# Optimization experiments

Measured on AMD Instinct MI355X. Metric: run time of the kernel, lower is better.

Reference implementation:

```python
import jax, jax.numpy as jnp
import numpy as np

EPS = 1e-6

def _ln(x, g, b):
    mu = x.mean(-1, keepdims=True)
    var = ((x - mu) ** 2).mean(-1, keepdims=True)
    return (x - mu) * jax.lax.rsqrt(var + EPS) * g + b

def _ln_l2_grad(z, target, g, b):
    # grad of 0.5*||LN(z)*g+b - target||^2 wrt z (fused L2/LayerNorm backward used by TTT)
    d = z.shape[-1]
    mu = z.mean(-1, keepdims=True)
    var = ((z - mu) ** 2).mean(-1, keepdims=True)
    std = jnp.sqrt(var + EPS)
    zh = (z - mu) / std
    go = (zh * g + b) - target
    gxh = go * g
    return (d * gxh - gxh.sum(-1, keepdims=True) - zh * (gxh * zh).sum(-1, keepdims=True)) / (d * std)

def _forward(x, W_down, b_down, Wq, Wk, Wv, Wo, W1, b1, ttt_g, ttt_b,
             lr_w, lr_b, post_g, post_b, norm_g, norm_b, W_up, b_up):
    B, S, D = x.shape
    A = W_down.shape[1]
    H, hd, _ = W1.shape
    # adapter down projection + SiLU
    h = jax.nn.silu(x @ W_down + b_down)                      # [B,S,A]
    # TTT-Linear: q/k/v projections split into heads
    xq = (h @ Wq).reshape(B, S, H, hd)
    xk = (h @ Wk).reshape(B, S, H, hd)
    xv = (h @ Wv).reshape(B, S, H, hd)
    eta = jax.nn.sigmoid(h @ lr_w + lr_b) / hd                # [B,S,H] token-wise learnable inner lr (base_lr=1)
    W1_0 = jnp.broadcast_to(W1, (B, H, hd, hd))
    b1_0 = jnp.broadcast_to(b1, (B, H, 1, hd))
    xs = (xq.transpose(1, 0, 2, 3), xk.transpose(1, 0, 2, 3),
          xv.transpose(1, 0, 2, 3), eta.transpose(1, 0, 2))

    def step(carry, ins):
        W, bb = carry                                         # [B,H,hd,hd], [B,H,1,hd]
        q, k, v, e = ins                                      # [B,H,hd] x3, [B,H]
        Z = jnp.einsum('bhd,bhde->bhe', k, W) + bb[:, :, 0, :]
        g = _ln_l2_grad(Z, v - k, ttt_g, ttt_b)               # inner-loop grad wrt pre-LN activations
        e4 = e[:, :, None, None]
        Wn = W - e4 * (k[..., :, None] * g[..., None, :])     # fast-weight SGD update
        bn = bb - e4 * g[:, :, None, :]
        Zq = jnp.einsum('bhd,bhde->bhe', q, Wn) + bn[:, :, 0, :]
        out = q + _ln(Zq, ttt_g, ttt_b)                       # per-head TTT post residual
        return (Wn, bn), out

    _, ys = jax.lax.scan(step, (W1_0, b1_0), xs)              # ys: [S,B,H,hd]
    t = ys.transpose(1, 0, 2, 3).reshape(B, S, A)
    t = _ln(t, post_g, post_b) @ Wo                           # TTT post-norm + output projection
    out = _ln(t, norm_g, norm_b)                              # adapter LayerNorm
    return out @ W_up + b_up                                  # adapter up projection (residual unused in source)

def setup_inputs() -> dict:
    key = jax.random.key(0)
    ks = jax.random.split(key, 12)
    B, S, D, A, H = 4, 1024, 768, 192, 3
    hd = A // H
    s = 0.02
    return {
        'x': jax.random.normal(ks[0], (B, S, D), jnp.float32),
        'W_down': jax.random.normal(ks[1], (D, A), jnp.float32) * s,
        'b_down': jnp.zeros((A,), jnp.float32),
        'Wq': jax.random.normal(ks[2], (A, A), jnp.float32) * s,
        'Wk': jax.random.normal(ks[3], (A, A), jnp.float32) * s,
        'Wv': jax.random.normal(ks[4], (A, A), jnp.float32) * s,
        'Wo': jax.random.normal(ks[5], (A, A), jnp.float32) * s,
        'W1': jax.random.normal(ks[6], (H, hd, hd), jnp.float32) * s,
        'b1': jnp.zeros((H, 1, hd), jnp.float32),
        'ttt_g': jnp.ones((H, hd), jnp.float32),
        'ttt_b': jnp.zeros((H, hd), jnp.float32),
        'lr_w': jax.random.normal(ks[7], (A, H), jnp.float32) * s,
        'lr_b': jnp.zeros((H,), jnp.float32),
        'post_g': jnp.ones((A,), jnp.float32),
        'post_b': jnp.zeros((A,), jnp.float32),
        'norm_g': jnp.ones((A,), jnp.float32),
        'norm_b': jnp.zeros((A,), jnp.float32),
        'W_up': jax.random.normal(ks[8], (A, D), jnp.float32) * s,
        'b_up': jnp.zeros((D,), jnp.float32),
    }

def reference(x, W_down, b_down, Wq, Wk, Wv, Wo, W1, b1, ttt_g, ttt_b,
              lr_w, lr_b, post_g, post_b, norm_g, norm_b, W_up, b_up):
    return _forward(x, W_down, b_down, Wq, Wk, Wv, Wo, W1, b1, ttt_g, ttt_b,
                    lr_w, lr_b, post_g, post_b, norm_g, norm_b, W_up, b_up)
```

## Files before the change

kernel.cpp:

```cpp
#include <hip/hip_runtime.h>
#include <hip/hip_bf16.h>
#include <math.h>

#define BDIM 4
#define SDIM 1024
#define DDIM 768
#define ADIM 192
#define HDIM 3
#define HD   64
#define MROWS (BDIM*SDIM)
#define NCHUNK (SDIM/32)
#define EPSLN 1e-6f

template<int CTRL, int RMASK, bool BC>
__device__ __forceinline__ float dpp_add_step(float x) {
    int t = __builtin_amdgcn_update_dpp(0, __float_as_int(x), CTRL, RMASK, 0xf, BC);
    return x + __int_as_float(t);
}
__device__ __forceinline__ float wave_bcast_sum(float x) {
    x = dpp_add_step<0x111, 0xf, true >(x);
    x = dpp_add_step<0x112, 0xf, true >(x);
    x = dpp_add_step<0x114, 0xf, true >(x);
    x = dpp_add_step<0x118, 0xf, true >(x);
    x = dpp_add_step<0x142, 0xa, false>(x);
    x = dpp_add_step<0x143, 0xc, false>(x);
    return __int_as_float(__builtin_amdgcn_readlane(__float_as_int(x), 63));
}
__device__ __forceinline__ float dpp_row16_sum(float x) {
    x = dpp_add_step<0x111, 0xf, true >(x);
    x = dpp_add_step<0x112, 0xf, true >(x);
    x = dpp_add_step<0x114, 0xf, true >(x);
    x = dpp_add_step<0x118, 0xf, true >(x);
    return x;
}
__device__ __forceinline__ float rl(float v, int lane) {
    return __int_as_float(__builtin_amdgcn_readlane(__float_as_int(v), lane));
}
__device__ __forceinline__ float fast_rsq(float x) {
    float r;
    asm("v_rsq_f32 %0, %1" : "=v"(r) : "v"(x));
    return r;
}
__device__ __forceinline__ void red5_asm(float& a, float& b, float& c,
                                         float& d, float& e) {
#define R5_SHR(N)                                                              \
    asm("v_add_f32 %0, %0, %0 row_shr:" #N " row_mask:0xf bank_mask:0xf bound_ctrl:0" : "+v"(a)); \
    asm("v_add_f32 %0, %0, %0 row_shr:" #N " row_mask:0xf bank_mask:0xf bound_ctrl:0" : "+v"(b)); \
    asm("v_add_f32 %0, %0, %0 row_shr:" #N " row_mask:0xf bank_mask:0xf bound_ctrl:0" : "+v"(c)); \
    asm("v_add_f32 %0, %0, %0 row_shr:" #N " row_mask:0xf bank_mask:0xf bound_ctrl:0" : "+v"(d)); \
    asm("v_add_f32 %0, %0, %0 row_shr:" #N " row_mask:0xf bank_mask:0xf bound_ctrl:0" : "+v"(e));
#define R5_BC(N, RM)                                                           \
    asm("v_add_f32 %0, %0, %0 row_bcast:" #N " row_mask:" #RM " bank_mask:0xf" : "+v"(a)); \
    asm("v_add_f32 %0, %0, %0 row_bcast:" #N " row_mask:" #RM " bank_mask:0xf" : "+v"(b)); \
    asm("v_add_f32 %0, %0, %0 row_bcast:" #N " row_mask:" #RM " bank_mask:0xf" : "+v"(c)); \
    asm("v_add_f32 %0, %0, %0 row_bcast:" #N " row_mask:" #RM " bank_mask:0xf" : "+v"(d)); \
    asm("v_add_f32 %0, %0, %0 row_bcast:" #N " row_mask:" #RM " bank_mask:0xf" : "+v"(e));
    R5_SHR(1) R5_SHR(2) R5_SHR(4) R5_SHR(8)
    R5_BC(15, 0xa) R5_BC(31, 0xc)
#undef R5_SHR
#undef R5_BC
}

template<int ACT, int LAYOUT, int LNA, int STATS>
__global__ __launch_bounds__(256) void gemm_k(
    const float* __restrict__ A, const float* __restrict__ Bm,
    const float* __restrict__ bias, float* __restrict__ C,
    int M, int N, int K,
    const float2* __restrict__ lnst, const float* __restrict__ lng,
    const float* __restrict__ lnbb, float2* __restrict__ ostat)
{
    __shared__ float As[16][68];
    __shared__ float Bs[16][68];
    __shared__ float2 lst[64];
    const int tid = threadIdx.x;
    const int bm = blockIdx.y * 64, bn = blockIdx.x * 64;
    const int tr = tid >> 4, tc = tid & 15;
    float acc[4][4] = {};

    if (LNA == 2) {
        if (tid < 64) {
            float2 s = lnst[bm + tid];
            float mu = s.x * (1.f / 192.f);
            float var = fmaf(-mu, mu, s.y * (1.f / 192.f));
            lst[tid] = make_float2(mu, rsqrtf(var + EPSLN));
        }
        __syncthreads();
    }

    for (int k0 = 0; k0 < K; k0 += 16) {
        #pragma unroll
        for (int p = 0; p < 4; ++p) {
            int m = (tid >> 4) + p * 16;
            int kk = tid & 15;
            float av = A[(size_t)(bm + m) * K + k0 + kk];
            if (LNA == 2) {
                float2 stv = lst[m];
                av = fmaf((av - stv.x) * stv.y, lng[k0 + kk], lnbb[k0 + kk]);
            }
            As[kk][m] = av;
        }
        #pragma unroll
        for (int p = 0; p < 4; ++p) {
            int kk = (tid >> 6) + p * 4;
            int n = tid & 63;
            Bs[kk][n] = Bm[(size_t)(k0 + kk) * N + bn + n];
        }
        __syncthreads();
        #pragma unroll
        for (int kk = 0; kk < 16; ++kk) {
            const float4 a4 = *(const float4*)&As[kk][tr * 4];
            const float4 b4 = *(const float4*)&Bs[kk][tc * 4];
            float aa[4] = {a4.x, a4.y, a4.z, a4.w};
            float bb[4] = {b4.x, b4.y, b4.z, b4.w};
            #pragma unroll
            for (int i = 0; i < 4; ++i)
                #pragma unroll
                for (int j = 0; j < 4; ++j)
                    acc[i][j] = fmaf(aa[i], bb[j], acc[i][j]);
        }
        __syncthreads();
    }

    float rs1[4] = {}, rs2[4] = {};
    #pragma unroll
    for (int i = 0; i < 4; ++i) {
        int m = bm + tr * 4 + i;
        #pragma unroll
        for (int j = 0; j < 4; ++j) {
            int n = bn + tc * 4 + j;
            float v = acc[i][j];
            if (bias) v += bias[n];
            if (ACT == 1) v = v / (1.f + __expf(-v));
            if (STATS) { rs1[i] += v; rs2[i] = fmaf(v, v, rs2[i]); }
            if (LAYOUT == 0) {
                C[(size_t)m * N + n] = v;
            } else {
                int b  = m >> 10, s = m & 1023;
                int hh = n >> 6,  d = n & 63;
                C[(((size_t)b * HDIM + hh) * SDIM + s) * HD + d] = v;
            }
        }
    }
    if (STATS) {
        #pragma unroll
        for (int i = 0; i < 4; ++i) {
            rs1[i] = dpp_row16_sum(rs1[i]);
            rs2[i] = dpp_row16_sum(rs2[i]);
        }
        if (tc == 15) {
            #pragma unroll
            for (int i = 0; i < 4; ++i) {
                atomicAdd(&ostat[bm + tr * 4 + i].x, rs1[i]);
                atomicAdd(&ostat[bm + tr * 4 + i].y, rs2[i]);
            }
        }
    }
}

__global__ __launch_bounds__(256) void gemm_qkv(
    const float* __restrict__ A, const float* __restrict__ BWq,
    const float* __restrict__ BWk, const float* __restrict__ BWv,
    float* __restrict__ Cbase)
{
    const float* Bm = (blockIdx.z == 0) ? BWq : (blockIdx.z == 1) ? BWk : BWv;
    float* C = Cbase + (size_t)blockIdx.z * ((size_t)MROWS * ADIM);
    __shared__ float As[16][68];
    __shared__ float Bs[16][68];
    const int tid = threadIdx.x;
    const int bm = blockIdx.y * 64, bn = blockIdx.x * 64;
    const int tr = tid >> 4, tc = tid & 15;
    float acc[4][4] = {};

    for (int k0 = 0; k0 < ADIM; k0 += 16) {
        #pragma unroll
        for (int p = 0; p < 4; ++p) {
            int m = (tid >> 4) + p * 16;
            int kk = tid & 15;
            As[kk][m] = A[(size_t)(bm + m) * ADIM + k0 + kk];
        }
        #pragma unroll
        for (int p = 0; p < 4; ++p) {
            int kk = (tid >> 6) + p * 4;
            int n = tid & 63;
            Bs[kk][n] = Bm[(size_t)(k0 + kk) * ADIM + bn + n];
        }
        __syncthreads();
        #pragma unroll
        for (int kk = 0; kk < 16; ++kk) {
            const float4 a4 = *(const float4*)&As[kk][tr * 4];
            const float4 b4 = *(const float4*)&Bs[kk][tc * 4];
            float aa[4] = {a4.x, a4.y, a4.z, a4.w};
            float bb[4] = {b4.x, b4.y, b4.z, b4.w};
            #pragma unroll
            for (int i = 0; i < 4; ++i)
                #pragma unroll
                for (int j = 0; j < 4; ++j)
                    acc[i][j] = fmaf(aa[i], bb[j], acc[i][j]);
        }
        __syncthreads();
    }

    #pragma unroll
    for (int i = 0; i < 4; ++i) {
        int m = bm + tr * 4 + i;
        #pragma unroll
        for (int j = 0; j < 4; ++j) {
            int n = bn + tc * 4 + j;
            int b  = m >> 10, s = m & 1023;
            int hh = n >> 6,  d = n & 63;
            C[(((size_t)b * HDIM + hh) * SDIM + s) * HD + d] = acc[i][j];
        }
    }
}

__global__ __launch_bounds__(256) void ab_kernel(
    const float* __restrict__ qb, const float* __restrict__ kb,
    float* __restrict__ vb,
    const float* __restrict__ ttt_g, const float* __restrict__ ttt_b,
    float* __restrict__ Ab, float* __restrict__ Bb,
    float* __restrict__ r6b,
    const float* __restrict__ h, const float* __restrict__ lr_w,
    const float* __restrict__ lr_b, float* __restrict__ etab,
    float4* __restrict__ stz)
{
    int bh = blockIdx.x >> 5, c = blockIdx.x & 31, cs = c * 32;
    int hh = bh % HDIM, b = bh / HDIM;
    __shared__ float Kc[32][65], Qc[32][65], Vc[32][65];
    __shared__ float ep[32][8];

    if (blockIdx.x < 16) {
        float4 z4; z4.x = z4.y = z4.z = z4.w = 0.f;
        stz[blockIdx.x * 256 + threadIdx.x] = z4;
    }

    {
        int rg = threadIdx.x >> 3, sl = threadIdx.x & 7;
        const float* hrow = h + ((size_t)b * SDIM + cs + rg) * ADIM + sl * 24;
        float esum = 0.f;
        #pragma unroll
        for (int jj = 0; jj < 24; ++jj)
            esum = fmaf(hrow[jj], lr_w[(sl * 24 + jj) * 3 + hh], esum);
        ep[rg][sl] = esum;
    }

    for (int i = threadIdx.x; i < 2048; i += 256) {
        int t = i >> 6, j = i & 63;
        Kc[t][j] = kb[((size_t)bh * SDIM + cs + t) * HD + j];
        Qc[t][j] = qb[((size_t)bh * SDIM + cs + t) * HD + j];
        Vc[t][j] = vb[((size_t)bh * SDIM + cs + t) * HD + j];
    }
    __syncthreads();

    if (threadIdx.x < 32) {
        int t = threadIdx.x;
        float acc = ((ep[t][0] + ep[t][1]) + (ep[t][2] + ep[t][3]))
                  + ((ep[t][4] + ep[t][5]) + (ep[t][6] + ep[t][7]))
                  + lr_b[hh];
        float e = 1.f / (1.f + __expf(-acc)) * (1.f / 64.f);
        etab[(size_t)bh * SDIM + cs + t] = e;
    }

    size_t base = ((size_t)(bh * NCHUNK + c)) * 1024;
    for (int e = threadIdx.x; e < 1024; e += 256) {
        int t = e >> 5, s = e & 31;
        float a = 1.f, bv = 1.f;
        #pragma unroll
        for (int j = 0; j < 64; ++j) {
            float ks = Kc[s][j];
            a  = fmaf(Kc[t][j], ks, a);
            bv = fmaf(Qc[t][j], ks, bv);
        }
        Ab[base + e] = a;
        Bb[base + e] = bv;
    }
    for (int i = threadIdx.x; i < 2048; i += 256) {
        int t = i >> 6, j = i & 63;
        float gwv = ttt_g[hh * 64 + j], bwv = ttt_b[hh * 64 + j];
        float av = fmaf(-(Vc[t][j] - Kc[t][j]), gwv, bwv * gwv);
        Vc[t][j] = av;
        vb[((size_t)bh * SDIM + cs + t) * HD + j] = av;
    }
    __syncthreads();
    if (threadIdx.x < 32) {
        int t = threadIdx.x;
        float acc = 0.f;
        #pragma unroll
        for (int j = 0; j < 64; ++j) acc += Vc[t][j];
        r6b[(size_t)bh * SDIM + cs + t] = acc;
    }
}

__device__ __forceinline__ void stage_chunk(
    int pp, int cc, int bh, int idx, int nth,
    const float* __restrict__ kbuf, const float* __restrict__ abuf,
    const float* __restrict__ Ab, const float* __restrict__ etab,
    const float* __restrict__ r6b,
    float4* K4, float4* a4, float4* A4, float2* er6)
{
    const float4* kg = (const float4*)(kbuf + ((size_t)bh * SDIM + cc * 32) * HD);
    const float4* ag = (const float4*)(abuf + ((size_t)bh * SDIM + cc * 32) * HD);
    const float4* Ag = (const float4*)(Ab + ((size_t)(bh * NCHUNK + cc)) * 1024);
    for (int i = idx; i < 512; i += nth) K4[pp * 512 + i] = kg[i];
    for (int i = idx; i < 512; i += nth) a4[pp * 512 + i] = ag[i];
    for (int i = idx; i < 256; i += nth) A4[pp * 256 + i] = Ag[i];
    for (int i = idx; i < 32; i += nth)
        er6[pp * 32 + i] = make_float2(
            etab[(size_t)bh * SDIM + cc * 32 + i] * (1.f / 64.f),
            r6b[(size_t)bh * SDIM + cc * 32 + i]);
}

__global__ __launch_bounds__(256, 1) void ttt_scan(
    const float* __restrict__ kbuf, const float* __restrict__ abuf,
    const float* __restrict__ etab, const float* __restrict__ Ab,
    const float* __restrict__ r6b,
    const float* __restrict__ W1,   const float* __restrict__ b1,
    const float* __restrict__ ttt_g, const float* __restrict__ ttt_b,
    float* __restrict__ Gbuf, float* __restrict__ W0save, float* __restrict__ b0save)
{
    const int bh = blockIdx.x, hh = bh % HDIM;
    const int tid = threadIdx.x, lane = tid & 63;
    const int wv = tid >> 6;
    __shared__ float  Zp[4][16][64];
    __shared__ float4 K4s[2 * 512];
    __shared__ float4 a4s[2 * 512];
    __shared__ float4 A4s[2 * 256];
    __shared__ float2 er6s[2 * 32];
    __shared__ float  Gl[16][64];

    float Wreg[16];
    #pragma unroll
    for (int r = 0; r < 16; ++r)
        Wreg[r] = W1[hh * 4096 + (wv * 16 + r) * 64 + lane];
    float breg = b1[hh * 64 + lane];
    const float gw = ttt_g[hh * 64 + lane];
    const float bw = ttt_b[hh * 64 + lane];
    const float w3 = gw * gw;
    (void)bw;
    const float Cg2 = wave_bcast_sum(w3);
    const float* a_f = (const float*)a4s;

    stage_chunk(0, 0, bh, tid, 256, kbuf, abuf, Ab, etab, r6b,
                K4s, a4s, A4s, er6s);
    __syncthreads();

    for (int c = 0; c < NCHUNK; ++c) {
        const int cs = c * 32;
        const int p = c & 1;

        {
            float* Wd = W0save + ((size_t)(bh * NCHUNK + c)) * 4096
                        + (wv * 16) * 64 + lane;
            #pragma unroll
            for (int r = 0; r < 16; ++r) Wd[r * 64] = Wreg[r];
            if (tid < 64) b0save[(bh * NCHUNK + c) * 64 + tid] = breg;
        }

        #pragma unroll
        for (int h = 0; h < 2; ++h) {
            const int h16 = h * 16, h4 = h * 4;

            float Zt[16];
            #pragma unroll
            for (int i = 0; i < 16; ++i) {
                const int t = h16 + i;
                float zt = 0.f;
                #pragma unroll
                for (int r4 = 0; r4 < 4; ++r4) {
                    const float4 kv = K4s[p * 512 + t * 16 + wv * 4 + r4];
                    zt = fmaf(kv.x, Wreg[r4 * 4 + 0], zt);
                    zt = fmaf(kv.y, Wreg[r4 * 4 + 1], zt);
                    zt = fmaf(kv.z, Wreg[r4 * 4 + 2], zt);
                    zt = fmaf(kv.w, Wreg[r4 * 4 + 3], zt);
                }
                Zt[i] = zt;
            }
            if (wv != 0) {
                #pragma unroll
                for (int i = 0; i < 16; ++i)
                    Zp[wv][i][lane] = (wv == 1) ? Zt[i] + breg : Zt[i];
            }
            __syncthreads();

            if (wv == 0) {
                __builtin_amdgcn_s_setprio(1);
                float Z[16];
                #pragma unroll
                for (int i = 0; i < 16; ++i) {
                    float q1 = Zp[1][i][lane], q2 = Zp[2][i][lane],
                          q3 = Zp[3][i][lane];
                    Z[i] = ((Zt[i] + q1) + (q2 + q3));
                }
                float4 avA[4], avB[4];
                float aA, aB; float2 erA, erB;
                #pragma unroll
                for (int q = 0; q < 4; ++q)
                    avA[q] = A4s[p * 256 + h16 * 8 + h4 + q];
                aA  = a_f[p * 2048 + h16 * 64 + lane];
                erA = er6s[p * 32 + h16];
#define TOK(I, avC, aC, erC, avN, aN, erN)                                     \
    {                                                                          \
        if ((I) < 15) {                                                        \
            _Pragma("unroll")                                                  \
            for (int q = ((I) + 2) >> 2; q < 4; ++q)                           \
                avN[q] = A4s[p * 256 + (h16 + (I) + 1) * 8 + h4 + q];          \
            aN  = a_f[p * 2048 + (h16 + (I) + 1) * 64 + lane];                 \
            erN = er6s[p * 32 + h16 + (I) + 1];                                \
        }                                                                      \
        float z  = Z[I];                                                       \
        float a  = aC;                                                         \
        float zg = z * w3;                                                     \
        float x1 = z, x2 = z * z, x3 = zg, x4 = zg * z, x5 = z * a;            \
        red5_asm(x1, x2, x3, x4, x5);                                          \
        float r1 = rl(x1, 63), r2 = rl(x2, 63), r3 = rl(x3, 63);               \
        float r4 = rl(x4, 63), r5 = rl(x5, 63);                                \
        float r6t = (erC).y;                                                   \
        float mu   = r1 * (1.f / 64.f);                                        \
        float var  = fmaf(-mu, mu, r2 * (1.f / 64.f));                         \
        float rstd = fast_rsq(var + EPSLN);                                    \
        float mc   = mu * Cg2;                                                 \
        float sgxh = fmaf(rstd, r3 - mc, r6t);                                 \
        float t4v  = fmaf(mu, mc, fmaf(-2.f * mu, r3, r4));                    \
        float sgz  = fmaf(rstd * rstd, t4v, rstd * (r5 - mu * r6t));           \
        float zh   = (z - mu) * rstd;                                          \
        float gxh  = fmaf(zh, w3, a);                                          \
        float ge   = (fmaf(64.f, gxh, -sgxh) - zh * sgz) * (rstd * (erC).x);   \
        Gl[I][lane] = ge;                                                      \
        _Pragma("unroll")                                                      \
        for (int u = (I) + 1; u < 16; ++u) {                                   \
            const float4 c4 = avC[(u) >> 2]; const int m4 = (u) & 3;           \
            float Atu = (m4 == 0) ? c4.x : (m4 == 1) ? c4.y                    \
                      : (m4 == 2) ? c4.z : c4.w;                               \
            Z[u] = fmaf(-Atu, ge, Z[u]);                                       \
        }                                                                      \
    }
                #pragma unroll
                for (int tp = 0; tp < 8; ++tp) {
                    TOK(2 * tp,     avA, aA, erA, avB, aB, erB)
                    TOK(2 * tp + 1, avB, aB, erB, avA, aA, erA)
                }
#undef TOK
                __builtin_amdgcn_s_setprio(0);
            } else if (h == 0 && c < NCHUNK - 1) {
                stage_chunk(p ^ 1, c + 1, bh, tid - 64, 192,
                            kbuf, abuf, Ab, etab, r6b, K4s, a4s, A4s, er6s);
            }
            __syncthreads();

            float btot = 0.f;
            #pragma unroll
            for (int s = 0; s < 16; ++s) {
                float gd = Gl[s][lane];
                btot += gd;
                #pragma unroll
                for (int r4 = 0; r4 < 4; ++r4) {
                    const float4 kv = K4s[p * 512 + (h16 + s) * 16 + wv * 4 + r4];
                    Wreg[r4 * 4 + 0] = fmaf(-kv.x, gd, Wreg[r4 * 4 + 0]);
                    Wreg[r4 * 4 + 1] = fmaf(-kv.y, gd, Wreg[r4 * 4 + 1]);
                    Wreg[r4 * 4 + 2] = fmaf(-kv.z, gd, Wreg[r4 * 4 + 2]);
                    Wreg[r4 * 4 + 3] = fmaf(-kv.w, gd, Wreg[r4 * 4 + 3]);
                }
            }
            breg -= btot;
            {
                float* gb = Gbuf + ((size_t)bh * SDIM + cs + h16) * HD + lane;
                #pragma unroll
                for (int r = 0; r < 4; ++r)
                    gb[(wv * 4 + r) * HD] = Gl[wv * 4 + r][lane];
            }
        }
    }
}

__global__ __launch_bounds__(256) void post_kernel(
    const float* __restrict__ qbuf, const float* __restrict__ Bb,
    const float* __restrict__ Gbuf, const float* __restrict__ W0save,
    const float* __restrict__ b0save,
    const float* __restrict__ ttt_g, const float* __restrict__ ttt_b,
    float* __restrict__ ys, float2* __restrict__ ystat)
{
    const int bh = blockIdx.x >> 5, c = blockIdx.x & 31, cs = c * 32;
    const int b = bh / HDIM, hh = bh % HDIM;
    const int tid = threadIdx.x, lane = tid & 63, wave = tid >> 6;
    __shared__ float Qc[32][65];
    __shared__ float W0l[64][65];
    __shared__ float Gl[32][64];
    for (int i = tid; i < 2048; i += 256) {
        int t = i >> 6, j = i & 63;
        Qc[t][j] = qbuf[((size_t)bh * SDIM + cs + t) * HD + j];
        Gl[t][j] = Gbuf[((size_t)bh * SDIM + cs + t) * HD + j];
    }
    for (int i = tid; i < 4096; i += 256)
        W0l[i >> 6][i & 63] = W0save[((size_t)(bh * NCHUNK + c)) * 4096 + i];
    __syncthreads();

    const float bb0 = b0save[(bh * NCHUNK + c) * 64 + lane];
    const float gw = ttt_g[hh * 64 + lane], bw = ttt_b[hh * 64 + lane];
    float acc[8];
    #pragma unroll
    for (int r = 0; r < 8; ++r) acc[r] = bb0;
    for (int j = 0; j < 64; ++j) {
        float w0 = W0l[j][lane];
        #pragma unroll
        for (int r = 0; r < 8; ++r)
            acc[r] = fmaf(Qc[wave * 8 + r][j], w0, acc[r]);
    }
    float Breg[8];
    size_t bbase = ((size_t)(bh * NCHUNK + c)) * 1024;
    #pragma unroll
    for (int r = 0; r < 8; ++r)
        Breg[r] = Bb[bbase + (wave * 8 + r) * 32 + (lane & 31)];
    #pragma unroll
    for (int s = 0; s < 32; ++s) {
        float gd = Gl[s][lane];
        #pragma unroll
        for (int r = 0; r < 8; ++r) {
            int t = wave * 8 + r;
            float Bts = rl(Breg[r], s);
            acc[r] = (s <= t) ? fmaf(-Bts, gd, acc[r]) : acc[r];
        }
    }
    #pragma unroll
    for (int r = 0; r < 8; ++r) {
        int t = wave * 8 + r;
        float s1 = wave_bcast_sum(acc[r]);
        float s2 = wave_bcast_sum(acc[r] * acc[r]);
        float mu = s1 * (1.f / 64.f);
        float var = s2 * (1.f / 64.f) - mu * mu;
        float rstd = rsqrtf(var + EPSLN);
        float zh = (acc[r] - mu) * rstd;
        float val = zh * gw + bw + Qc[t][lane];
        ys[((size_t)(b * SDIM) + cs + t) * ADIM + hh * HD + lane] = val;
        float t1 = wave_bcast_sum(val);
        float t2 = wave_bcast_sum(val * val);
        if (lane == 0) {
            atomicAdd(&ystat[(size_t)b * SDIM + cs + t].x, t1);
            atomicAdd(&ystat[(size_t)b * SDIM + cs + t].y, t2);
        }
    }
}

extern "C" void kernel_launch(void* const* d_in, const int* in_sizes, int n_in,
                              void* d_out, int out_size, void* d_ws, size_t ws_size,
                              hipStream_t stream)
{
    const float* x      = (const float*)d_in[0];
    const float* W_down = (const float*)d_in[1];
    const float* b_down = (const float*)d_in[2];
    const float* Wq     = (const float*)d_in[3];
    const float* Wk     = (const float*)d_in[4];
    const float* Wv     = (const float*)d_in[5];
    const float* Wo     = (const float*)d_in[6];
    const float* W1     = (const float*)d_in[7];
    const float* b1     = (const float*)d_in[8];
    const float* ttt_g  = (const float*)d_in[9];
    const float* ttt_b  = (const float*)d_in[10];
    const float* lr_w   = (const float*)d_in[11];
    const float* lr_b   = (const float*)d_in[12];
    const float* post_g = (const float*)d_in[13];
    const float* post_b = (const float*)d_in[14];
    const float* norm_g = (const float*)d_in[15];
    const float* norm_b = (const float*)d_in[16];
    const float* W_up   = (const float*)d_in[17];
    const float* b_up   = (const float*)d_in[18];
    float* out = (float*)d_out;

    float* ws = (float*)d_ws;
    const size_t SZ = (size_t)MROWS * ADIM;
    float* h    = ws;
    float* qb   = ws + SZ;
    float* kb   = ws + 2 * SZ;
    float* vb   = ws + 3 * SZ;
    float* Gb   = ws + 4 * SZ;
    float* etab = ws + 5 * SZ;
    float* Ab   = etab + 12288;
    float* Bb   = Ab + 393216;
    float* W0s  = Bb + 393216;
    float* b0s  = W0s + 1572864;
    float* r6b  = b0s + 24576;
    float2* ystat = (float2*)(r6b + 12288);
    float2* tstat = ystat + 4096;
    float* ysb  = h;
    float* tbuf = qb;

    gemm_k<1, 0, 0, 0><<<dim3(ADIM / 64, MROWS / 64), 256, 0, stream>>>(
        x, W_down, b_down, h, MROWS, ADIM, DDIM,
        nullptr, nullptr, nullptr, nullptr);
    gemm_qkv<<<dim3(ADIM / 64, MROWS / 64, 3), 256, 0, stream>>>(
        h, Wq, Wk, Wv, qb);
    ab_kernel<<<BDIM * HDIM * NCHUNK, 256, 0, stream>>>(
        qb, kb, vb, ttt_g, ttt_b, Ab, Bb, r6b,
        h, lr_w, lr_b, etab, (float4*)ystat);
    ttt_scan<<<BDIM * HDIM, 256, 0, stream>>>(
        kb, vb, etab, Ab, r6b, W1, b1, ttt_g, ttt_b, Gb, W0s, b0s);
    post_kernel<<<BDIM * HDIM * NCHUNK, 256, 0, stream>>>(
        qb, Bb, Gb, W0s, b0s, ttt_g, ttt_b, ysb, ystat);
    gemm_k<0, 0, 2, 1><<<dim3(ADIM / 64, MROWS / 64), 256, 0, stream>>>(
        ysb, Wo, nullptr, tbuf, MROWS, ADIM, ADIM,
        ystat, post_g, post_b, tstat);
    gemm_k<0, 0, 2, 0><<<dim3(DDIM / 64, MROWS / 64), 256, 0, stream>>>(
        tbuf, W_up, b_up, out, MROWS, DDIM, ADIM,
        tstat, norm_g, norm_b, nullptr);
}
```

Measured before the change: 455.3 us.

## Run dense projection GEMMs on bf16 MFMA with pre-transposed bf16 weights

All the dense GEMMs (down, q/k/v, Wo, up) switch from fp32 FMA tiles to bf16 MFMA 16x16x32 instructions. Activations are converted to bf16 while they are staged into shared memory. A new wconv kernel transposes each weight matrix to bf16 in the workspace on every call. This targets the FMA-bound GEMM time, which is likely a modest share next to the sequential TTT scan. It costs bf16 rounding error and one extra launch.

```diff
diff --git a/kernel.cpp b/kernel.cpp
--- a/kernel.cpp
+++ b/kernel.cpp
@@ -12,6 +12,9 @@
 #define NCHUNK (SDIM/32)
 #define EPSLN 1e-6f
 
+typedef __attribute__((ext_vector_type(8))) short bf16x8;
+typedef __attribute__((ext_vector_type(4))) float f32x4;
+
 template<int CTRL, int RMASK, bool BC>
 __device__ __forceinline__ float dpp_add_step(float x) {
     int t = __builtin_amdgcn_update_dpp(0, __float_as_int(x), CTRL, RMASK, 0xf, BC);
@@ -40,6 +43,11 @@
     float r;
     asm("v_rsq_f32 %0, %1" : "=v"(r) : "v"(x));
     return r;
+}
+__device__ __forceinline__ unsigned short f2bf(float f) {
+    unsigned int u = __float_as_uint(f);
+    u += 0x7fffu + ((u >> 16) & 1u);
+    return (unsigned short)(u >> 16);
 }
 __device__ __forceinline__ void red5_asm(float& a, float& b, float& c,
                                          float& d, float& e) {
@@ -61,21 +69,52 @@
 #undef R5_BC
 }
 
+__global__ __launch_bounds__(256) void wconv(
+    const float* __restrict__ w0, unsigned short* __restrict__ o0,
+    const float* __restrict__ w1, unsigned short* __restrict__ o1,
+    const float* __restrict__ w2, unsigned short* __restrict__ o2,
+    const float* __restrict__ w3, unsigned short* __restrict__ o3,
+    const float* __restrict__ w4, unsigned short* __restrict__ o4,
+    const float* __restrict__ w5, unsigned short* __restrict__ o5)
+{
+    int z = blockIdx.z;
+    const float* in; unsigned short* outp; int K, N;
+    if      (z == 0) { in = w0; outp = o0; K = DDIM; N = ADIM; }
+    else if (z == 1) { in = w1; outp = o1; K = ADIM; N = ADIM; }
+    else if (z == 2) { in = w2; outp = o2; K = ADIM; N = ADIM; }
+    else if (z == 3) { in = w3; outp = o3; K = ADIM; N = ADIM; }
+    else if (z == 4) { in = w4; outp = o4; K = ADIM; N = ADIM; }
+    else             { in = w5; outp = o5; K = ADIM; N = DDIM; }
+    int bk = blockIdx.x * 32, bn = blockIdx.y * 32;
+    if (bk >= K || bn >= N) return;
+    __shared__ float t[32][33];
+    int tk = threadIdx.x & 31, tn = threadIdx.x >> 5;
+    #pragma unroll
+    for (int r = 0; r < 4; ++r)
+        t[tn + r * 8][tk] = in[(size_t)(bk + tn + r * 8) * N + bn + tk];
+    __syncthreads();
+    #pragma unroll
+    for (int r = 0; r < 4; ++r)
+        outp[(size_t)(bn + tn + r * 8) * K + bk + tk] = f2bf(t[tk][tn + r * 8]);
+}
+
 template<int ACT, int LAYOUT, int LNA, int STATS>
 __global__ __launch_bounds__(256) void gemm_k(
-    const float* __restrict__ A, const float* __restrict__ Bm,
+    const float* __restrict__ A, const unsigned short* __restrict__ Bt,
     const float* __restrict__ bias, float* __restrict__ C,
     int M, int N, int K,
     const float2* __restrict__ lnst, const float* __restrict__ lng,
     const float* __restrict__ lnbb, float2* __restrict__ ostat)
 {
-    __shared__ float As[16][68];
-    __shared__ float Bs[16][68];
+    __shared__ unsigned short As[64][40];
+    __shared__ unsigned short Bs[64][40];
     __shared__ float2 lst[64];
     const int tid = threadIdx.x;
     const int bm = blockIdx.y * 64, bn = blockIdx.x * 64;
-    const int tr = tid >> 4, tc = tid & 15;
-    float acc[4][4] = {};
+    const int lane = tid & 63, wv = tid >> 6;
+    const int wr = wv >> 1, wc = wv & 1;
+    const int l15 = lane & 15, l4 = lane >> 4;
+    f32x4 acc[2][2] = {};
 
     if (LNA == 2) {
         if (tid < 64) {
@@ -87,130 +126,140 @@
         __syncthreads();
     }
 
-    for (int k0 = 0; k0 < K; k0 += 16) {
-        #pragma unroll
-        for (int p = 0; p < 4; ++p) {
-            int m = (tid >> 4) + p * 16;
-            int kk = tid & 15;
-            float av = A[(size_t)(bm + m) * K + k0 + kk];
+    const int sm = tid >> 2;
+    const int sk = (tid & 3) * 8;
+    for (int k0 = 0; k0 < K; k0 += 32) {
+        {
+            const float* ap = A + (size_t)(bm + sm) * K + k0 + sk;
+            float4 a0 = *(const float4*)ap;
+            float4 a1 = *(const float4*)(ap + 4);
+            float av[8] = {a0.x, a0.y, a0.z, a0.w, a1.x, a1.y, a1.z, a1.w};
             if (LNA == 2) {
-                float2 stv = lst[m];
-                av = fmaf((av - stv.x) * stv.y, lng[k0 + kk], lnbb[k0 + kk]);
-            }
-            As[kk][m] = av;
-        }
-        #pragma unroll
-        for (int p = 0; p < 4; ++p) {
-            int kk = (tid >> 6) + p * 4;
-            int n = tid & 63;
-            Bs[kk][n] = Bm[(size_t)(k0 + kk) * N + bn + n];
+                float2 stv = lst[sm];
+                #pragma unroll
+                for (int e = 0; e < 8; ++e)
+                    av[e] = fmaf((av[e] - stv.x) * stv.y,
+                                 lng[k0 + sk + e], lnbb[k0 + sk + e]);
+            }
+            uint4 w;
+            w.x = (unsigned)f2bf(av[0]) | ((unsigned)f2bf(av[1]) << 16);
+            w.y = (unsigned)f2bf(av[2]) | ((unsigned)f2bf(av[3]) << 16);
+            w.z = (unsigned)f2bf(av[4]) | ((unsigned)f2bf(av[5]) << 16);
+            w.w = (unsigned)f2bf(av[6]) | ((unsigned)f2bf(av[7]) << 16);
+            *(uint4*)&As[sm][sk] = w;
+        }
+        {
+            *(uint4*)&Bs[sm][sk] =
+                *(const uint4*)(Bt + (size_t)(bn + sm) * K + k0 + sk);
         }
         __syncthreads();
-        #pragma unroll
-        for (int kk = 0; kk < 16; ++kk) {
-            const float4 a4 = *(const float4*)&As[kk][tr * 4];
-            const float4 b4 = *(const float4*)&Bs[kk][tc * 4];
-            float aa[4] = {a4.x, a4.y, a4.z, a4.w};
-            float bb[4] = {b4.x, b4.y, b4.z, b4.w};
+        bf16x8 af0 = *(const bf16x8*)&As[wr * 32 + l15][l4 * 8];
+        bf16x8 af1 = *(const bf16x8*)&As[wr * 32 + 16 + l15][l4 * 8];
+        bf16x8 bf0 = *(const bf16x8*)&Bs[wc * 32 + l15][l4 * 8];
+        bf16x8 bf1 = *(const bf16x8*)&Bs[wc * 32 + 16 + l15][l4 * 8];
+        acc[0][0] = __builtin_amdgcn_mfma_f32_16x16x32_bf16(af0, bf0, acc[0][0], 0, 0, 0);
+        acc[0][1] = __builtin_amdgcn_mfma_f32_16x16x32_bf16(af0, bf1, acc[0][1], 0, 0, 0);
+        acc[1][0] = __builtin_amdgcn_mfma_f32_16x16x32_bf16(af1, bf0, acc[1][0], 0, 0, 0);
+        acc[1][1] = __builtin_amdgcn_mfma_f32_16x16x32_bf16(af1, bf1, acc[1][1], 0, 0, 0);
+        __syncthreads();
+    }
+
+    float rs1[2][4] = {}, rs2[2][4] = {};
+    #pragma unroll
+    for (int rt = 0; rt < 2; ++rt) {
+        #pragma unroll
+        for (int ct = 0; ct < 2; ++ct) {
             #pragma unroll
-            for (int i = 0; i < 4; ++i)
-                #pragma unroll
-                for (int j = 0; j < 4; ++j)
-                    acc[i][j] = fmaf(aa[i], bb[j], acc[i][j]);
-        }
+            for (int r = 0; r < 4; ++r) {
+                int m = bm + wr * 32 + rt * 16 + l4 * 4 + r;
+                int n = bn + wc * 32 + ct * 16 + l15;
+                float v = acc[rt][ct][r];
+                if (bias) v += bias[n];
+                if (ACT == 1) v = v / (1.f + __expf(-v));
+                if (STATS) { rs1[rt][r] += v; rs2[rt][r] = fmaf(v, v, rs2[rt][r]); }
+                if (LAYOUT == 0) {
+                    C[(size_t)m * N + n] = v;
+                } else {
+                    int b  = m >> 10, s = m & 1023;
+                    int hh = n >> 6,  d = n & 63;
+                    C[(((size_t)b * HDIM + hh) * SDIM + s) * HD + d] = v;
+                }
+            }
+        }
+    }
+    if (STATS) {
+        #pragma unroll
+        for (int rt = 0; rt < 2; ++rt)
+            #pragma unroll
+            for (int r = 0; r < 4; ++r) {
+                float s1 = dpp_row16_sum(rs1[rt][r]);
+                float s2 = dpp_row16_sum(rs2[rt][r]);
+                if (l15 == 15) {
+                    int m = bm + wr * 32 + rt * 16 + l4 * 4 + r;
+                    atomicAdd(&ostat[m].x, s1);
+                    atomicAdd(&ostat[m].y, s2);
+                }
+            }
+    }
+}
+
+__global__ __launch_bounds__(256) void gemm_qkv(
+    const float* __restrict__ A, const unsigned short* __restrict__ BTq,
+    const unsigned short* __restrict__ BTk, const unsigned short* __restrict__ BTv,
+    float* __restrict__ Cbase)
+{
+    const unsigned short* Bt = (blockIdx.z == 0) ? BTq
+                              : (blockIdx.z == 1) ? BTk : BTv;
+    float* C = Cbase + (size_t)blockIdx.z * ((size_t)MROWS * ADIM);
+    __shared__ unsigned short As[64][40];
+    __shared__ unsigned short Bs[64][40];
+    const int tid = threadIdx.x;
+    const int bm = blockIdx.y * 64, bn = blockIdx.x * 64;
+    const int lane = tid & 63, wv = tid >> 6;
+    const int wr = wv >> 1, wc = wv & 1;
+    const int l15 = lane & 15, l4 = lane >> 4;
+    f32x4 acc[2][2] = {};
+
+    const int sm = tid >> 2;
+    const int sk = (tid & 3) * 8;
+    for (int k0 = 0; k0 < ADIM; k0 += 32) {
+        {
+            const float* ap = A + (size_t)(bm + sm) * ADIM + k0 + sk;
+            float4 a0 = *(const float4*)ap;
+            float4 a1 = *(const float4*)(ap + 4);
+            uint4 w;
+            w.x = (unsigned)f2bf(a0.x) | ((unsigned)f2bf(a0.y) << 16);
+            w.y = (unsigned)f2bf(a0.z) | ((unsigned)f2bf(a0.w) << 16);
+            w.z = (unsigned)f2bf(a1.x) | ((unsigned)f2bf(a1.y) << 16);
+            w.w = (unsigned)f2bf(a1.z) | ((unsigned)f2bf(a1.w) << 16);
+            *(uint4*)&As[sm][sk] = w;
+        }
+        *(uint4*)&Bs[sm][sk] =
+            *(const uint4*)(Bt + (size_t)(bn + sm) * ADIM + k0 + sk);
         __syncthreads();
-    }
-
-    float rs1[4] = {}, rs2[4] = {};
-    #pragma unroll
-    for (int i = 0; i < 4; ++i) {
-        int m = bm + tr * 4 + i;
-        #pragma unroll
-        for (int j = 0; j < 4; ++j) {
-            int n = bn + tc * 4 + j;
-            float v = acc[i][j];
-            if (bias) v += bias[n];
-            if (ACT == 1) v = v / (1.f + __expf(-v));
-            if (STATS) { rs1[i] += v; rs2[i] = fmaf(v, v, rs2[i]); }
-            if (LAYOUT == 0) {
-                C[(size_t)m * N + n] = v;
-            } else {
+        bf16x8 af0 = *(const bf16x8*)&As[wr * 32 + l15][l4 * 8];
+        bf16x8 af1 = *(const bf16x8*)&As[wr * 32 + 16 + l15][l4 * 8];
+        bf16x8 bf0 = *(const bf16x8*)&Bs[wc * 32 + l15][l4 * 8];
+        bf16x8 bf1 = *(const bf16x8*)&Bs[wc * 32 + 16 + l15][l4 * 8];
+        acc[0][0] = __builtin_amdgcn_mfma_f32_16x16x32_bf16(af0, bf0, acc[0][0], 0, 0, 0);
+        acc[0][1] = __builtin_amdgcn_mfma_f32_16x16x32_bf16(af0, bf1, acc[0][1], 0, 0, 0);
+        acc[1][0] = __builtin_amdgcn_mfma_f32_16x16x32_bf16(af1, bf0, acc[1][0], 0, 0, 0);
+        acc[1][1] = __builtin_amdgcn_mfma_f32_16x16x32_bf16(af1, bf1, acc[1][1], 0, 0, 0);
+        __syncthreads();
+    }
+
+    #pragma unroll
+    for (int rt = 0; rt < 2; ++rt)
+        #pragma unroll
+        for (int ct = 0; ct < 2; ++ct)
+            #pragma unroll
+            for (int r = 0; r < 4; ++r) {
+                int m = bm + wr * 32 + rt * 16 + l4 * 4 + r;
+                int n = bn + wc * 32 + ct * 16 + l15;
                 int b  = m >> 10, s = m & 1023;
                 int hh = n >> 6,  d = n & 63;
-                C[(((size_t)b * HDIM + hh) * SDIM + s) * HD + d] = v;
-            }
-        }
-    }
-    if (STATS) {
-        #pragma unroll
-        for (int i = 0; i < 4; ++i) {
-            rs1[i] = dpp_row16_sum(rs1[i]);
-            rs2[i] = dpp_row16_sum(rs2[i]);
-        }
-        if (tc == 15) {
-            #pragma unroll
-            for (int i = 0; i < 4; ++i) {
-                atomicAdd(&ostat[bm + tr * 4 + i].x, rs1[i]);
-                atomicAdd(&ostat[bm + tr * 4 + i].y, rs2[i]);
-            }
-        }
-    }
-}
-
-__global__ __launch_bounds__(256) void gemm_qkv(
-    const float* __restrict__ A, const float* __restrict__ BWq,
-    const float* __restrict__ BWk, const float* __restrict__ BWv,
-    float* __restrict__ Cbase)
-{
-    const float* Bm = (blockIdx.z == 0) ? BWq : (blockIdx.z == 1) ? BWk : BWv;
-    float* C = Cbase + (size_t)blockIdx.z * ((size_t)MROWS * ADIM);
-    __shared__ float As[16][68];
-    __shared__ float Bs[16][68];
-    const int tid = threadIdx.x;
-    const int bm = blockIdx.y * 64, bn = blockIdx.x * 64;
-    const int tr = tid >> 4, tc = tid & 15;
-    float acc[4][4] = {};
-
-    for (int k0 = 0; k0 < ADIM; k0 += 16) {
-        #pragma unroll
-        for (int p = 0; p < 4; ++p) {
-            int m = (tid >> 4) + p * 16;
-            int kk = tid & 15;
-            As[kk][m] = A[(size_t)(bm + m) * ADIM + k0 + kk];
-        }
-        #pragma unroll
-        for (int p = 0; p < 4; ++p) {
-            int kk = (tid >> 6) + p * 4;
-            int n = tid & 63;
-            Bs[kk][n] = Bm[(size_t)(k0 + kk) * ADIM + bn + n];
-        }
-        __syncthreads();
-        #pragma unroll
-        for (int kk = 0; kk < 16; ++kk) {
-            const float4 a4 = *(const float4*)&As[kk][tr * 4];
-            const float4 b4 = *(const float4*)&Bs[kk][tc * 4];
-            float aa[4] = {a4.x, a4.y, a4.z, a4.w};
-            float bb[4] = {b4.x, b4.y, b4.z, b4.w};
-            #pragma unroll
-            for (int i = 0; i < 4; ++i)
-                #pragma unroll
-                for (int j = 0; j < 4; ++j)
-                    acc[i][j] = fmaf(aa[i], bb[j], acc[i][j]);
-        }
-        __syncthreads();
-    }
-
-    #pragma unroll
-    for (int i = 0; i < 4; ++i) {
-        int m = bm + tr * 4 + i;
-        #pragma unroll
-        for (int j = 0; j < 4; ++j) {
-            int n = bn + tc * 4 + j;
-            int b  = m >> 10, s = m & 1023;
-            int hh = n >> 6,  d = n & 63;
-            C[(((size_t)b * HDIM + hh) * SDIM + s) * HD + d] = acc[i][j];
-        }
-    }
+                C[(((size_t)b * HDIM + hh) * SDIM + s) * HD + d] = acc[rt][ct][r];
+            }
 }
 
 __global__ __launch_bounds__(256) void ab_kernel(
@@ -579,14 +628,22 @@
     float* r6b  = b0s + 24576;
     float2* ystat = (float2*)(r6b + 12288);
     float2* tstat = ystat + 4096;
+    unsigned short* WdT = (unsigned short*)(tstat + 4096);
+    unsigned short* WqT = WdT + 147456;
+    unsigned short* WkT = WqT + 36864;
+    unsigned short* WvT = WkT + 36864;
+    unsigned short* WoT = WvT + 36864;
+    unsigned short* WuT = WoT + 36864;
     float* ysb  = h;
     float* tbuf = qb;
 
+    wconv<<<dim3(24, 24, 6), 256, 0, stream>>>(
+        W_down, WdT, Wq, WqT, Wk, WkT, Wv, WvT, Wo, WoT, W_up, WuT);
     gemm_k<1, 0, 0, 0><<<dim3(ADIM / 64, MROWS / 64), 256, 0, stream>>>(
-        x, W_down, b_down, h, MROWS, ADIM, DDIM,
+        x, WdT, b_down, h, MROWS, ADIM, DDIM,
         nullptr, nullptr, nullptr, nullptr);
     gemm_qkv<<<dim3(ADIM / 64, MROWS / 64, 3), 256, 0, stream>>>(
-        h, Wq, Wk, Wv, qb);
+        h, WqT, WkT, WvT, qb);
     ab_kernel<<<BDIM * HDIM * NCHUNK, 256, 0, stream>>>(
         qb, kb, vb, ttt_g, ttt_b, Ab, Bb, r6b,
         h, lr_w, lr_b, etab, (float4*)ystat);
@@ -595,9 +652,9 @@
     post_kernel<<<BDIM * HDIM * NCHUNK, 256, 0, stream>>>(
         qb, Bb, Gb, W0s, b0s, ttt_g, ttt_b, ysb, ystat);
     gemm_k<0, 0, 2, 1><<<dim3(ADIM / 64, MROWS / 64), 256, 0, stream>>>(
-        ysb, Wo, nullptr, tbuf, MROWS, ADIM, ADIM,
+        ysb, WoT, nullptr, tbuf, MROWS, ADIM, ADIM,
         ystat, post_g, post_b, tstat);
     gemm_k<0, 0, 2, 0><<<dim3(DDIM / 64, MROWS / 64), 256, 0, stream>>>(
-        tbuf, W_up, b_up, out, MROWS, DDIM, ADIM,
+        tbuf, WuT, b_up, out, MROWS, DDIM, ADIM,
         tstat, norm_g, norm_b, nullptr);
 }
```

Result: faster. 402.6 us (-11.6%).
